# Performance work log

Hardware: AMD Instinct MI355X
Metric: run time of the kernel (lower is better)

## Reference

```python
import jax, jax.numpy as jnp
import numpy as np

N = 50000   # nodes per graph
F = 128     # num_features (== hidden width 128 in GCNConv stack)
G = 3       # number_graphs
E = 600000  # edges per graph


def setup_inputs() -> dict:
    key = jax.random.key(0)
    ks = jax.random.split(key, 16)
    s = 0.05  # glorot-ish scale for 128-wide layers
    inp = {
        "x": jax.random.normal(ks[0], (G, N, F), jnp.float32),
        "fc1_w": jax.random.normal(ks[1], (G, F, F), jnp.float32) * s,
        "fc1_b": jnp.zeros((G, F), jnp.float32),
        "w_conv1": jax.random.normal(ks[2], (F, 128), jnp.float32) * s,
        "b_conv1": jnp.zeros((128,), jnp.float32),
        "w_conv2": jax.random.normal(ks[3], (128, 128), jnp.float32) * s,
        "b_conv2": jnp.zeros((128,), jnp.float32),
        "w_dconv1": jax.random.normal(ks[4], (128, 128), jnp.float32) * s,
        "b_dconv1": jnp.zeros((128,), jnp.float32),
        "w_dconv2": jax.random.normal(ks[5], (128, F), jnp.float32) * s,
        "b_dconv2": jnp.zeros((F,), jnp.float32),
        "fc2_w": jax.random.normal(ks[6], (2 * F, F), jnp.float32) * s,
        "fc2_b": jnp.zeros((F,), jnp.float32),
        "att_w": jax.random.normal(ks[7], (G, 128, 128), jnp.float32) * s,
        "edge_index": jax.random.randint(ks[8], (G, 2, E), 0, N, jnp.int64),
    }
    return inp


def _gcn(x, src, dst, W, b):
    # PyG GCNConv: add self-loops, symmetric D^-1/2 (A+I) D^-1/2 normalization
    n = x.shape[0]
    h = x @ W                                  # [N, out]
    loops = jnp.arange(n)
    s = jnp.concatenate([src, loops])
    d = jnp.concatenate([dst, loops])
    deg = jax.ops.segment_sum(jnp.ones_like(d, dtype=h.dtype), d, num_segments=n)
    dinv = jnp.where(deg > 0, jax.lax.rsqrt(deg), 0.0)
    norm = dinv[s] * dinv[d]                   # [E+N]
    out = jax.ops.segment_sum(h[s] * norm[:, None], d, num_segments=n)
    return out + b


_gcn_g = jax.vmap(_gcn, in_axes=(0, 0, 0, None, None))  # over graphs (shared weights)


def _fro(a):
    # Frobenius norm over last two axes (matches torch.norm(., p=2) on a matrix)
    return jnp.sqrt(jnp.sum(a * a, axis=(-2, -1)))


def reference(x, fc1_w, fc1_b, w_conv1, b_conv1, w_conv2, b_conv2,
              w_dconv1, b_dconv1, w_dconv2, b_dconv2, fc2_w, fc2_b,
              att_w, edge_index):
    g = x.shape[0]
    src, dst = edge_index[:, 0], edge_index[:, 1]

    # per-graph fc1 (distinct weights per graph)
    pre_feat = jnp.einsum('gnf,gfo->gno', x, fc1_w) + fc1_b[:, None, :]
    conv1_f = _gcn_g(pre_feat, src, dst, w_conv1, b_conv1)   # [G,N,128]
    enc = _gcn_g(conv1_f, src, dst, w_conv2, b_conv2)        # encoder_H [G,N,128]

    global_vec = jax.nn.sigmoid(jnp.mean(enc, axis=1))       # [G,128]

    # leave-one-out decoder input: (sum_j enc_j - enc_i) / (G-1)
    dec_in = (jnp.sum(enc, axis=0)[None] - enc) / (g - 1)

    own1 = _gcn_g(enc, src, dst, w_dconv1, b_dconv1)         # decov1_f
    own2 = _gcn_g(own1, src, dst, w_dconv2, b_dconv2)        # reconstructed x
    oth1 = _gcn_g(dec_in, src, dst, w_dconv1, b_dconv1)
    oth2 = _gcn_g(oth1, src, dst, w_dconv2, b_dconv2)

    fuse_h = jnp.concatenate([own2, oth2], axis=-1)          # [G,N,2F]
    each_fin = jnp.einsum('gnf,fo->gno', fuse_h, fc2_w) + fc2_b  # [G,N,F]

    # cross-graph attention: sigmoid(H_j @ W_i @ g_i) for all (i, j)
    u = jnp.einsum('ide,ie->id', att_w, global_vec)          # W_i @ g_i -> [G,128]
    S = jax.nn.sigmoid(jnp.einsum('jnd,id->ijn', enc, u))    # [i,j,n]
    L = jnp.transpose(S, (0, 2, 1))                          # [i,n,j]
    L = L / jnp.sum(L, axis=-1, keepdims=True)               # row-normalize over j
    comp_re = jnp.transpose(L, (1, 0, 2)).reshape(x.shape[1], g * g)  # [N, G*G]

    fuse_feat = jax.nn.sigmoid(jnp.mean(each_fin, axis=0))   # [N,F]
    used_feat = jax.nn.elu(jnp.mean(enc, axis=0))            # [N,128]

    obf1 = jnp.sum((_fro(pre_feat - own2) + _fro(conv1_f - own1)) / 2)
    obf0 = jnp.float32(0.0)
    for i in range(g):
        for j in range(g):
            if i != j:
                obf0 = obf0 + _fro(each_fin[i] - each_fin[j])
    return (fuse_feat, used_feat, comp_re, obf1, obf0)
```

## Files before the change

kernel.cpp:

```cpp
#include <hip/hip_runtime.h>

#define NN 50000
#define NFEAT 128
#define NG 3
#define NE 600000

typedef unsigned int u32;
typedef unsigned short u16;
typedef __bf16 bf16x8 __attribute__((ext_vector_type(8)));
typedef float f32x4 __attribute__((ext_vector_type(4)));

__device__ __forceinline__ u16 f2bf(float f){
  u32 u = __float_as_uint(f);
  return (u16)((u + 0x7fffu + ((u >> 16) & 1u)) >> 16);
}
__device__ __forceinline__ float bf2f(u32 s){
  return __uint_as_float((s & 0xffffu) << 16);
}
__device__ __forceinline__ u32 pack2(float a, float b){
  return (u32)f2bf(a) | ((u32)f2bf(b) << 16);
}
__device__ __forceinline__ float sigm(float x){ return 1.f / (1.f + __expf(-x)); }

__global__ void wprep_kernel(const float* fc1w, const float* wc1, const float* wc2,
                             const float* wd1, const float* wd2, const float* fc2w,
                             u16* WT){
  int idx = blockIdx.x * 256 + threadIdx.x;
  if (idx >= 147456) return;
  float v;
  if (idx < 49152){
    int g = idx / 16384, r = idx % 16384; int o = r / 128, f = r % 128;
    v = fc1w[g * 16384 + f * 128 + o];
  } else if (idx < 114688){
    int m = (idx - 49152) / 16384, r = (idx - 49152) % 16384;
    int o = r / 128, f = r % 128;
    const float* w = (m == 0) ? wc1 : (m == 1) ? wc2 : (m == 2) ? wd1 : wd2;
    v = w[f * 128 + o];
  } else {
    int r = idx - 114688; int half = r / 16384; r %= 16384;
    int o = r / 128, f = r % 128;
    v = fc2w[(half * 128 + f) * 128 + o];
  }
  WT[idx] = f2bf(v);
}

__global__ void deg_kernel(const int* ei, int* deg){
  int t = blockIdx.x * 256 + threadIdx.x;
  if (t >= NG * NE) return;
  int g = t / NE, e = t - g * NE;
  int dst = ei[(size_t)g * 2 * NE + NE + e];
  atomicAdd(deg + (size_t)g * NN + dst, 1);
}

__global__ __launch_bounds__(1024) void scan_kernel(const int* deg, int* rowptr, float* dinv){
  const int g = blockIdx.x;
  const int* d = deg + (size_t)g * NN;
  int* rp = rowptr + g * (NN + 1);
  float* di = dinv + (size_t)g * NN;
  __shared__ int s[1024];
  __shared__ int carry;
  if (threadIdx.x == 0) carry = 0;
  __syncthreads();
  for (int base = 0; base <= NN; base += 1024){
    int idx = base + threadIdx.x;
    int v = (idx < NN) ? d[idx] : 0;
    if (idx < NN) di[idx] = rsqrtf((float)(v + 1));
    s[threadIdx.x] = v;
    __syncthreads();
    for (int off = 1; off < 1024; off <<= 1){
      int x = (threadIdx.x >= off) ? s[threadIdx.x - off] : 0;
      __syncthreads();
      s[threadIdx.x] += x;
      __syncthreads();
    }
    int incl = s[threadIdx.x];
    int run = carry;
    if (idx <= NN) rp[idx] = run + incl - v;
    __syncthreads();
    if (threadIdx.x == 1023) carry = run + s[1023];
    __syncthreads();
  }
}

__global__ void fill_kernel(const int* ei, const int* rowptr, int* cursor, int* colbuf){
  int t = blockIdx.x * 256 + threadIdx.x;
  if (t >= NG * NE) return;
  int g = t / NE, e = t - g * NE;
  int src = ei[(size_t)g * 2 * NE + e];
  int dst = ei[(size_t)g * 2 * NE + NE + e];
  int pos = atomicAdd(cursor + (size_t)g * NN + dst, 1);
  colbuf[(size_t)g * NE + rowptr[g * (NN + 1) + dst] + pos] = src;
}

template<int MODE>
__global__ __launch_bounds__(256, 2) void gemm_kernel(
    const void* Ap, const void* Ap2, const u16* W, const u16* W2,
    const float* bias, u16* Out, int wPerG, int biasPerG, int hasBias)
{
  __shared__ __align__(16) unsigned char sA[128 * 256];
  __shared__ __align__(16) unsigned char sW[128 * 256];
  const int tid = threadIdx.x;
  const int g = blockIdx.y;
  const int nb = blockIdx.x * 128;
  const int lane = tid & 63, wv = tid >> 6;
  const int wm = (wv & 1) * 64, wn = (wv >> 1) * 64;
  const int l15 = lane & 15, lh = lane >> 4;
  f32x4 acc[4][4] = {};
  constexpr int passes = (MODE == 3) ? 2 : 1;
  for (int p = 0; p < passes; p++){
    if (p) __syncthreads();
    {
      const u16* wsrc = (p ? W2 : W) + (wPerG ? g * 16384 : 0);
      const uint4* w4 = (const uint4*)wsrc;
      for (int i = tid; i < 2048; i += 256){
        int r = i >> 4, c = i & 15;
        uint4 v = w4[i];
        *(uint4*)(sW + r * 256 + ((c * 16) ^ ((r & 7) << 4))) = v;
      }
    }
    if (MODE == 1){
      const float* xp = (const float*)Ap + (size_t)g * NN * NFEAT;
      for (int i = tid; i < 2048; i += 256){
        int r = i >> 4, c = i & 15; int node = nb + r;
        uint4 o = {0, 0, 0, 0};
        if (node < NN){
          const float* row = xp + (size_t)node * NFEAT + c * 8;
          float4 a4 = *(const float4*)row;
          float4 b4 = *(const float4*)(row + 4);
          o.x = pack2(a4.x, a4.y); o.y = pack2(a4.z, a4.w);
          o.z = pack2(b4.x, b4.y); o.w = pack2(b4.z, b4.w);
        }
        *(uint4*)(sA + r * 256 + ((c * 16) ^ ((r & 7) << 4))) = o;
      }
    } else if (MODE == 2){
      const uint4* pe = (const uint4*)((const u16*)Ap + (size_t)g * NN * NFEAT);
      const uint4* ps = (const uint4*)Ap2;
      for (int i = tid; i < 2048; i += 256){
        int r = i >> 4, c = i & 15; int node = nb + r;
        uint4 o = {0, 0, 0, 0};
        if (node < NN){
          uint4 va = pe[(size_t)node * 16 + c];
          uint4 vb = ps[(size_t)node * 16 + c];
          o.x = pack2(0.5f * (bf2f(vb.x) - bf2f(va.x)), 0.5f * (bf2f(vb.x >> 16) - bf2f(va.x >> 16)));
          o.y = pack2(0.5f * (bf2f(vb.y) - bf2f(va.y)), 0.5f * (bf2f(vb.y >> 16) - bf2f(va.y >> 16)));
          o.z = pack2(0.5f * (bf2f(vb.z) - bf2f(va.z)), 0.5f * (bf2f(vb.z >> 16) - bf2f(va.z >> 16)));
          o.w = pack2(0.5f * (bf2f(vb.w) - bf2f(va.w)), 0.5f * (bf2f(vb.w >> 16) - bf2f(va.w >> 16)));
        }
        *(uint4*)(sA + r * 256 + ((c * 16) ^ ((r & 7) << 4))) = o;
      }
    } else {
      const u16* asrc = (const u16*)(p ? Ap2 : Ap) + (size_t)g * NN * NFEAT;
      const uint4* a4 = (const uint4*)asrc;
      for (int i = tid; i < 2048; i += 256){
        int r = i >> 4, c = i & 15; int node = nb + r;
        uint4 v = {0, 0, 0, 0};
        if (node < NN) v = a4[(size_t)node * 16 + c];
        *(uint4*)(sA + r * 256 + ((c * 16) ^ ((r & 7) << 4))) = v;
      }
    }
    __syncthreads();
    #pragma unroll
    for (int k0 = 0; k0 < 128; k0 += 32){
      const int kb = 2 * (k0 + lh * 8);
      bf16x8 af[4], bfr[4];
      #pragma unroll
      for (int t = 0; t < 4; t++){
        int rm = wm + t * 16 + l15;
        af[t] = *reinterpret_cast<const bf16x8*>(sW + rm * 256 + (kb ^ ((rm & 7) << 4)));
        int rn = wn + t * 16 + l15;
        bfr[t] = *reinterpret_cast<const bf16x8*>(sA + rn * 256 + (kb ^ ((rn & 7) << 4)));
      }
      #pragma unroll
      for (int mi = 0; mi < 4; mi++)
        #pragma unroll
        for (int ni = 0; ni < 4; ni++)
          acc[mi][ni] = __builtin_amdgcn_mfma_f32_16x16x32_bf16(af[mi], bfr[ni], acc[mi][ni], 0, 0, 0);
    }
  }
  u16* outg = Out + (size_t)g * NN * NFEAT;
  #pragma unroll
  for (int mi = 0; mi < 4; mi++){
    int mbase = wm + mi * 16 + lh * 4;
    f32x4 bv = {};
    if (hasBias) bv = *reinterpret_cast<const f32x4*>(bias + (biasPerG ? g * NFEAT : 0) + mbase);
    #pragma unroll
    for (int ni = 0; ni < 4; ni++){
      int node = nb + wn + ni * 16 + l15;
      if (node < NN){
        f32x4 v = acc[mi][ni];
        ushort4 o;
        o.x = f2bf(v.x + bv.x); o.y = f2bf(v.y + bv.y);
        o.z = f2bf(v.z + bv.z); o.w = f2bf(v.w + bv.w);
        *reinterpret_cast<ushort4*>(outg + (size_t)node * NFEAT + mbase) = o;
      }
    }
  }
}

template<bool SQ>
__global__ __launch_bounds__(256) void agg_kernel(
    const u16* H, u16* Outp, const float* bias, const float* dinv,
    const int* rowptr, const int* colidx, const u16* Ref, float* sqslot)
{
  __shared__ float red[256];
  const int g = blockIdx.y;
  const int v = blockIdx.x * 4 + (threadIdx.x >> 6);
  const int l = threadIdx.x & 63;
  const u32* h = (const u32*)(H + (size_t)g * NN * NFEAT);
  const float* dv = dinv + (size_t)g * NN;
  const int* rp = rowptr + g * (NN + 1);
  const int* ci = colidx + (size_t)g * NE;
  float ax = 0.f, ay = 0.f;
  const int e0 = rp[v], e1 = rp[v + 1];
  int e = e0;
  for (; e + 1 < e1; e += 2){
    int s0 = ci[e], s1 = ci[e + 1];
    float w0 = dv[s0], w1 = dv[s1];
    u32 h0 = h[(size_t)s0 * 64 + l], h1 = h[(size_t)s1 * 64 + l];
    ax += w0 * bf2f(h0) + w1 * bf2f(h1);
    ay += w0 * bf2f(h0 >> 16) + w1 * bf2f(h1 >> 16);
  }
  if (e < e1){
    int s0 = ci[e]; float w0 = dv[s0];
    u32 h0 = h[(size_t)s0 * 64 + l];
    ax += w0 * bf2f(h0); ay += w0 * bf2f(h0 >> 16);
  }
  const float dvv = dv[v];
  u32 hs = h[(size_t)v * 64 + l];
  ax = (ax + dvv * bf2f(hs)) * dvv;
  ay = (ay + dvv * bf2f(hs >> 16)) * dvv;
  const float2 b2 = *(const float2*)(bias + 2 * l);
  ax += b2.x; ay += b2.y;
  ((u32*)(Outp + (size_t)g * NN * NFEAT))[(size_t)v * 64 + l] = pack2(ax, ay);
  if (SQ){
    u32 rv = ((const u32*)(Ref + (size_t)g * NN * NFEAT))[(size_t)v * 64 + l];
    float dx = bf2f(rv) - ax, dy = bf2f(rv >> 16) - ay;
    red[threadIdx.x] = dx * dx + dy * dy;
    __syncthreads();
    for (int s2 = 128; s2 > 0; s2 >>= 1){
      if (threadIdx.x < s2) red[threadIdx.x] += red[threadIdx.x + s2];
      __syncthreads();
    }
    if (threadIdx.x == 0) atomicAdd(sqslot + g, red[0]);
  }
}

__global__ __launch_bounds__(256) void encsum_kernel(
    const u16* Enc, u16* EncSum, float* outUsed, float* colsum)
{
  const int fp = threadIdx.x & 63, sub = threadIdx.x >> 6;
  const u32* e0 = (const u32*)Enc;
  const u32* e1 = e0 + (size_t)NN * 64;
  const u32* e2 = e1 + (size_t)NN * 64;
  u32* es = (u32*)EncSum;
  float cs[6] = {0, 0, 0, 0, 0, 0};
  for (int v = blockIdx.x * 4 + sub; v < NN; v += gridDim.x * 4){
    size_t idx = (size_t)v * 64 + fp;
    u32 a = e0[idx], b = e1[idx], c = e2[idx];
    float axv = bf2f(a), ayv = bf2f(a >> 16);
    float bxv = bf2f(b), byv = bf2f(b >> 16);
    float cxv = bf2f(c), cyv = bf2f(c >> 16);
    cs[0] += axv; cs[1] += ayv; cs[2] += bxv; cs[3] += byv; cs[4] += cxv; cs[5] += cyv;
    float sx = axv + bxv + cxv, sy = ayv + byv + cyv;
    es[idx] = pack2(sx, sy);
    float ux = sx * (1.f / 3.f), uy = sy * (1.f / 3.f);
    float2 o;
    o.x = ux > 0.f ? ux : expm1f(ux);
    o.y = uy > 0.f ? uy : expm1f(uy);
    *(float2*)(outUsed + (size_t)v * NFEAT + 2 * fp) = o;
  }
  __shared__ float red[256];
  #pragma unroll
  for (int q = 0; q < 6; q++){
    red[threadIdx.x] = cs[q];
    __syncthreads();
    if (sub == 0){
      float s = red[fp] + red[64 + fp] + red[128 + fp] + red[192 + fp];
      atomicAdd(&colsum[(q >> 1) * NFEAT + 2 * fp + (q & 1)], s);
    }
    __syncthreads();
  }
}

__global__ void gvecu_kernel(const float* colsum, const float* att, float* u){
  __shared__ float gv[3 * 128];
  const int t = threadIdx.x;
  for (int g = 0; g < 3; g++) gv[g * 128 + t] = sigm(colsum[g * 128 + t] * (1.f / 50000.f));
  __syncthreads();
  for (int i = 0; i < 3; i++){
    float s = 0.f;
    for (int e = 0; e < 128; e++)
      s += att[(size_t)i * 16384 + (size_t)t * 128 + e] * gv[i * 128 + e];
    u[i * 128 + t] = s;
  }
}

__global__ __launch_bounds__(256) void fuse_kernel(const u16* EF, float* outFuse, float* slots){
  const int fp = threadIdx.x & 63, sub = threadIdx.x >> 6;
  const u32* e0 = (const u32*)EF;
  const u32* e1 = e0 + (size_t)NN * 64;
  const u32* e2 = e1 + (size_t)NN * 64;
  float s01 = 0, s02 = 0, s12 = 0;
  for (int v = blockIdx.x * 4 + sub; v < NN; v += gridDim.x * 4){
    size_t idx = (size_t)v * 64 + fp;
    u32 a = e0[idx], b = e1[idx], c = e2[idx];
    float axv = bf2f(a), ayv = bf2f(a >> 16), bxv = bf2f(b), byv = bf2f(b >> 16);
    float cxv = bf2f(c), cyv = bf2f(c >> 16);
    float2 o;
    o.x = sigm((axv + bxv + cxv) * (1.f / 3.f));
    o.y = sigm((ayv + byv + cyv) * (1.f / 3.f));
    *(float2*)(outFuse + (size_t)v * NFEAT + 2 * fp) = o;
    float dx, dy;
    dx = axv - bxv; dy = ayv - byv; s01 += dx * dx + dy * dy;
    dx = axv - cxv; dy = ayv - cyv; s02 += dx * dx + dy * dy;
    dx = bxv - cxv; dy = byv - cyv; s12 += dx * dx + dy * dy;
  }
  __shared__ float red[256];
  float vals[3] = {s01, s02, s12};
  #pragma unroll
  for (int q = 0; q < 3; q++){
    red[threadIdx.x] = vals[q];
    __syncthreads();
    for (int s2 = 128; s2 > 0; s2 >>= 1){
      if (threadIdx.x < s2) red[threadIdx.x] += red[threadIdx.x + s2];
      __syncthreads();
    }
    if (threadIdx.x == 0) atomicAdd(slots + 6 + q, red[0]);
    __syncthreads();
  }
}

__global__ __launch_bounds__(256) void comp_kernel(const u16* Enc, const float* u, float* outC){
  __shared__ float su[384];
  for (int i = threadIdx.x; i < 384; i += 256) su[i] = u[i];
  __syncthreads();
  const int v = blockIdx.x * 4 + (threadIdx.x >> 6);
  const int l = threadIdx.x & 63;
  const u32* e = (const u32*)Enc;
  float ex[3], ey[3];
  #pragma unroll
  for (int j = 0; j < 3; j++){
    u32 t = e[((size_t)j * NN + v) * 64 + l];
    ex[j] = bf2f(t); ey[j] = bf2f(t >> 16);
  }
  float p[9];
  #pragma unroll
  for (int i = 0; i < 3; i++){
    float uxi = su[i * 128 + 2 * l], uyi = su[i * 128 + 2 * l + 1];
    #pragma unroll
    for (int j = 0; j < 3; j++)
      p[i * 3 + j] = ex[j] * uxi + ey[j] * uyi;
  }
  #pragma unroll
  for (int q = 0; q < 9; q++){
    float s = p[q];
    #pragma unroll
    for (int off = 1; off < 64; off <<= 1) s += __shfl_xor(s, off, 64);
    p[q] = s;
  }
  if (l < 9){
    float sg[9];
    #pragma unroll
    for (int q = 0; q < 9; q++) sg[q] = sigm(p[q]);
    float d0 = sg[0] + sg[1] + sg[2], d1 = sg[3] + sg[4] + sg[5], d2 = sg[6] + sg[7] + sg[8];
    float num = sg[0];
    if (l == 1) num = sg[1]; if (l == 2) num = sg[2]; if (l == 3) num = sg[3];
    if (l == 4) num = sg[4]; if (l == 5) num = sg[5]; if (l == 6) num = sg[6];
    if (l == 7) num = sg[7]; if (l == 8) num = sg[8];
    float den = (l < 3) ? d0 : (l < 6) ? d1 : d2;
    outC[(size_t)v * 9 + l] = num / den;
  }
}

__global__ void final_kernel(const float* slots, float* out){
  if (threadIdx.x == 0){
    float obf1 = 0.f;
    for (int g = 0; g < 3; g++)
      obf1 += 0.5f * (sqrtf(slots[3 + g]) + sqrtf(slots[g]));
    float obf0 = 2.f * (sqrtf(slots[6]) + sqrtf(slots[7]) + sqrtf(slots[8]));
    out[13250000] = obf1;
    out[13250001] = obf0;
  }
}

extern "C" void kernel_launch(void* const* d_in, const int* in_sizes, int n_in,
                              void* d_out, int out_size, void* d_ws, size_t ws_size,
                              hipStream_t stream)
{
  (void)in_sizes; (void)n_in; (void)out_size;
  const float* x    = (const float*)d_in[0];
  const float* fc1w = (const float*)d_in[1];
  const float* fc1b = (const float*)d_in[2];
  const float* wc1  = (const float*)d_in[3];
  const float* bc1  = (const float*)d_in[4];
  const float* wc2  = (const float*)d_in[5];
  const float* bc2  = (const float*)d_in[6];
  const float* wd1  = (const float*)d_in[7];
  const float* bd1  = (const float*)d_in[8];
  const float* wd2  = (const float*)d_in[9];
  const float* bd2  = (const float*)d_in[10];
  const float* fc2w = (const float*)d_in[11];
  const float* fc2b = (const float*)d_in[12];
  const float* attw = (const float*)d_in[13];
  const int*   ei   = (const int*)d_in[14];
  float* out = (float*)d_out;
  char* ws = (char*)d_ws;

  constexpr size_t BUFB = (size_t)NG * NN * NFEAT * 2;
  u16* WT   = (u16*)(ws + 0);
  u16* buf0 = (u16*)(ws + 327680);
  u16* buf1 = (u16*)(ws + 327680 + 1 * BUFB);
  u16* buf2 = (u16*)(ws + 327680 + 2 * BUFB);
  u16* buf3 = (u16*)(ws + 327680 + 3 * BUFB);
  u16* buf4 = (u16*)(ws + 327680 + 4 * BUFB);
  u16* buf5 = (u16*)(ws + 327680 + 5 * BUFB);
  size_t off = 327680 + 6 * BUFB;
  u16* encsum = (u16*)(ws + off); off += (size_t)NN * NFEAT * 2;
  float* dinv = (float*)(ws + off); off += (size_t)NG * NN * 4;
  int* rowptr = (int*)(ws + off); off += 600064;
  int* colbuf = (int*)(ws + off); off += (size_t)NG * NE * 4;
  size_t zero_off = off;
  int* deg     = (int*)(ws + off); off += (size_t)NG * NN * 4;
  int* cursor  = (int*)(ws + off); off += (size_t)NG * NN * 4;
  float* colsum = (float*)(ws + off); off += 1536;
  float* slots  = (float*)(ws + off); off += 64;
  size_t zero_bytes = off - zero_off;
  float* uvec = (float*)(ws + off); off += 1536;
  if (ws_size < off) return;

  hipMemsetAsync(ws + zero_off, 0, zero_bytes, stream);

  wprep_kernel<<<576, 256, 0, stream>>>(fc1w, wc1, wc2, wd1, wd2, fc2w, WT);
  deg_kernel<<<7032, 256, 0, stream>>>(ei, deg);
  scan_kernel<<<NG, 1024, 0, stream>>>(deg, rowptr, dinv);
  fill_kernel<<<7032, 256, 0, stream>>>(ei, rowptr, cursor, colbuf);

  const u16* WT_fc1 = WT;
  const u16* WT_c1  = WT + 49152;
  const u16* WT_c2  = WT + 65536;
  const u16* WT_d1  = WT + 81920;
  const u16* WT_d2  = WT + 98304;
  const u16* WT_f2a = WT + 114688;
  const u16* WT_f2b = WT + 131072;
  dim3 gg(391, NG), ag(12500, NG);

  gemm_kernel<1><<<gg, 256, 0, stream>>>(x, nullptr, WT_fc1, nullptr, fc1b, buf0, 1, 1, 1);
  gemm_kernel<0><<<gg, 256, 0, stream>>>(buf0, nullptr, WT_c1, nullptr, nullptr, buf3, 0, 0, 0);
  agg_kernel<false><<<ag, 256, 0, stream>>>(buf3, buf1, bc1, dinv, rowptr, colbuf, nullptr, nullptr);
  gemm_kernel<0><<<gg, 256, 0, stream>>>(buf1, nullptr, WT_c2, nullptr, nullptr, buf3, 0, 0, 0);
  agg_kernel<false><<<ag, 256, 0, stream>>>(buf3, buf2, bc2, dinv, rowptr, colbuf, nullptr, nullptr);
  encsum_kernel<<<256, 256, 0, stream>>>(buf2, encsum, out + 6400000, colsum);
  gvecu_kernel<<<1, 128, 0, stream>>>(colsum, attw, uvec);
  gemm_kernel<0><<<gg, 256, 0, stream>>>(buf2, nullptr, WT_d1, nullptr, nullptr, buf3, 0, 0, 0);
  agg_kernel<true><<<ag, 256, 0, stream>>>(buf3, buf4, bd1, dinv, rowptr, colbuf, buf1, slots + 0);
  gemm_kernel<0><<<gg, 256, 0, stream>>>(buf4, nullptr, WT_d2, nullptr, nullptr, buf3, 0, 0, 0);
  agg_kernel<true><<<ag, 256, 0, stream>>>(buf3, buf5, bd2, dinv, rowptr, colbuf, buf0, slots + 3);
  gemm_kernel<2><<<gg, 256, 0, stream>>>(buf2, encsum, WT_d1, nullptr, nullptr, buf3, 0, 0, 0);
  agg_kernel<false><<<ag, 256, 0, stream>>>(buf3, buf1, bd1, dinv, rowptr, colbuf, nullptr, nullptr);
  gemm_kernel<0><<<gg, 256, 0, stream>>>(buf1, nullptr, WT_d2, nullptr, nullptr, buf3, 0, 0, 0);
  agg_kernel<false><<<ag, 256, 0, stream>>>(buf3, buf4, bd2, dinv, rowptr, colbuf, nullptr, nullptr);
  gemm_kernel<3><<<gg, 256, 0, stream>>>(buf5, buf4, WT_f2a, WT_f2b, fc2b, buf0, 0, 0, 1);
  fuse_kernel<<<256, 256, 0, stream>>>(buf0, out, slots);
  comp_kernel<<<12500, 256, 0, stream>>>(buf2, uvec, out + 12800000);
  final_kernel<<<1, 64, 0, stream>>>(slots, out);
}
```

Measured before the change: 2.235 ms.

## Pre-scale GEMM output by source dinv and vectorize edge aggregation with uint4 gathers

The GEMM epilogue now multiplies each node's row by its dinv, so the aggregation kernel no longer gathers a per-edge dinv[src] weight and only sums pre-scaled rows. The aggregation is restructured so each wavefront processes 8 neighbours at a time, with 16 lanes per row reading uint4 (8 bf16) chunks, followed by a cross-lane shuffle reduction. The SQ reduction uses wave shuffles and a 4-entry shared array instead of a full 256-entry tree. This trades an extra bf16 rounding of pre-scaled values and some idle lanes on low-degree nodes for fewer dependent loads and wider memory transactions.

```diff
diff --git a/kernel.cpp b/kernel.cpp
--- a/kernel.cpp
+++ b/kernel.cpp
@@ -95,7 +95,8 @@
 template<int MODE>
 __global__ __launch_bounds__(256, 2) void gemm_kernel(
     const void* Ap, const void* Ap2, const u16* W, const u16* W2,
-    const float* bias, u16* Out, int wPerG, int biasPerG, int hasBias)
+    const float* bias, u16* Out, const float* scale,
+    int wPerG, int biasPerG, int hasBias)
 {
   __shared__ __align__(16) unsigned char sA[128 * 256];
   __shared__ __align__(16) unsigned char sW[128 * 256];
@@ -177,6 +178,15 @@
           acc[mi][ni] = __builtin_amdgcn_mfma_f32_16x16x32_bf16(af[mi], bfr[ni], acc[mi][ni], 0, 0, 0);
     }
   }
+  float scn[4] = {1.f, 1.f, 1.f, 1.f};
+  if (scale){
+    const float* sg = scale + (size_t)g * NN;
+    #pragma unroll
+    for (int ni = 0; ni < 4; ni++){
+      int node = nb + wn + ni * 16 + l15;
+      scn[ni] = (node < NN) ? sg[node] : 0.f;
+    }
+  }
   u16* outg = Out + (size_t)g * NN * NFEAT;
   #pragma unroll
   for (int mi = 0; mi < 4; mi++){
@@ -188,9 +198,10 @@
       int node = nb + wn + ni * 16 + l15;
       if (node < NN){
         f32x4 v = acc[mi][ni];
+        float s = scn[ni];
         ushort4 o;
-        o.x = f2bf(v.x + bv.x); o.y = f2bf(v.y + bv.y);
-        o.z = f2bf(v.z + bv.z); o.w = f2bf(v.w + bv.w);
+        o.x = f2bf((v.x + bv.x) * s); o.y = f2bf((v.y + bv.y) * s);
+        o.z = f2bf((v.z + bv.z) * s); o.w = f2bf((v.w + bv.w) * s);
         *reinterpret_cast<ushort4*>(outg + (size_t)node * NFEAT + mbase) = o;
       }
     }
@@ -202,46 +213,75 @@
     const u16* H, u16* Outp, const float* bias, const float* dinv,
     const int* rowptr, const int* colidx, const u16* Ref, float* sqslot)
 {
-  __shared__ float red[256];
   const int g = blockIdx.y;
   const int v = blockIdx.x * 4 + (threadIdx.x >> 6);
   const int l = threadIdx.x & 63;
-  const u32* h = (const u32*)(H + (size_t)g * NN * NFEAT);
-  const float* dv = dinv + (size_t)g * NN;
+  const int q = l >> 4, sub = l & 15;
+  const uint4* h4 = (const uint4*)(H + (size_t)g * NN * NFEAT);
   const int* rp = rowptr + g * (NN + 1);
   const int* ci = colidx + (size_t)g * NE;
-  float ax = 0.f, ay = 0.f;
-  const int e0 = rp[v], e1 = rp[v + 1];
-  int e = e0;
-  for (; e + 1 < e1; e += 2){
-    int s0 = ci[e], s1 = ci[e + 1];
-    float w0 = dv[s0], w1 = dv[s1];
-    u32 h0 = h[(size_t)s0 * 64 + l], h1 = h[(size_t)s1 * 64 + l];
-    ax += w0 * bf2f(h0) + w1 * bf2f(h1);
-    ay += w0 * bf2f(h0 >> 16) + w1 * bf2f(h1 >> 16);
-  }
-  if (e < e1){
-    int s0 = ci[e]; float w0 = dv[s0];
-    u32 h0 = h[(size_t)s0 * 64 + l];
-    ax += w0 * bf2f(h0); ay += w0 * bf2f(h0 >> 16);
-  }
-  const float dvv = dv[v];
-  u32 hs = h[(size_t)v * 64 + l];
-  ax = (ax + dvv * bf2f(hs)) * dvv;
-  ay = (ay + dvv * bf2f(hs >> 16)) * dvv;
-  const float2 b2 = *(const float2*)(bias + 2 * l);
-  ax += b2.x; ay += b2.y;
-  ((u32*)(Outp + (size_t)g * NN * NFEAT))[(size_t)v * 64 + l] = pack2(ax, ay);
+  const int e0 = rp[v];
+  const int nslot = rp[v + 1] - e0 + 1;
+  float a0=0,a1=0,a2=0,a3=0,a4=0,a5=0,a6=0,a7=0;
+  const int nIter = (nslot + 7) >> 3;
+  for (int it = 0; it < nIter; ++it){
+    int sA = it * 8 + q;
+    int sB = sA + 4;
+    int srcA = (sA == 0) ? v : ((sA < nslot) ? ci[e0 + sA - 1] : v);
+    int srcB = (sB < nslot) ? ci[e0 + sB - 1] : v;
+    uint4 hA = h4[(size_t)srcA * 16 + sub];
+    uint4 hB = h4[(size_t)srcB * 16 + sub];
+    if (sA < nslot){
+      a0 += bf2f(hA.x); a1 += bf2f(hA.x >> 16);
+      a2 += bf2f(hA.y); a3 += bf2f(hA.y >> 16);
+      a4 += bf2f(hA.z); a5 += bf2f(hA.z >> 16);
+      a6 += bf2f(hA.w); a7 += bf2f(hA.w >> 16);
+    }
+    if (sB < nslot){
+      a0 += bf2f(hB.x); a1 += bf2f(hB.x >> 16);
+      a2 += bf2f(hB.y); a3 += bf2f(hB.y >> 16);
+      a4 += bf2f(hB.z); a5 += bf2f(hB.z >> 16);
+      a6 += bf2f(hB.w); a7 += bf2f(hB.w >> 16);
+    }
+  }
+  a0 += __shfl_xor(a0, 16); a1 += __shfl_xor(a1, 16);
+  a2 += __shfl_xor(a2, 16); a3 += __shfl_xor(a3, 16);
+  a4 += __shfl_xor(a4, 16); a5 += __shfl_xor(a5, 16);
+  a6 += __shfl_xor(a6, 16); a7 += __shfl_xor(a7, 16);
+  a0 += __shfl_xor(a0, 32); a1 += __shfl_xor(a1, 32);
+  a2 += __shfl_xor(a2, 32); a3 += __shfl_xor(a3, 32);
+  a4 += __shfl_xor(a4, 32); a5 += __shfl_xor(a5, 32);
+  a6 += __shfl_xor(a6, 32); a7 += __shfl_xor(a7, 32);
+  const float dvv = dinv[(size_t)g * NN + v];
+  const float4 b4a = *(const float4*)(bias + sub * 8);
+  const float4 b4b = *(const float4*)(bias + sub * 8 + 4);
+  a0 = a0 * dvv + b4a.x; a1 = a1 * dvv + b4a.y;
+  a2 = a2 * dvv + b4a.z; a3 = a3 * dvv + b4a.w;
+  a4 = a4 * dvv + b4b.x; a5 = a5 * dvv + b4b.y;
+  a6 = a6 * dvv + b4b.z; a7 = a7 * dvv + b4b.w;
+  float sq = 0.f;
+  if (q == 0){
+    uint4 o;
+    o.x = pack2(a0, a1); o.y = pack2(a2, a3);
+    o.z = pack2(a4, a5); o.w = pack2(a6, a7);
+    ((uint4*)(Outp + (size_t)g * NN * NFEAT))[(size_t)v * 16 + sub] = o;
+    if (SQ){
+      uint4 rv = ((const uint4*)(Ref + (size_t)g * NN * NFEAT))[(size_t)v * 16 + sub];
+      float d;
+      d = bf2f(rv.x) - a0; sq += d * d; d = bf2f(rv.x >> 16) - a1; sq += d * d;
+      d = bf2f(rv.y) - a2; sq += d * d; d = bf2f(rv.y >> 16) - a3; sq += d * d;
+      d = bf2f(rv.z) - a4; sq += d * d; d = bf2f(rv.z >> 16) - a5; sq += d * d;
+      d = bf2f(rv.w) - a6; sq += d * d; d = bf2f(rv.w >> 16) - a7; sq += d * d;
+    }
+  }
   if (SQ){
-    u32 rv = ((const u32*)(Ref + (size_t)g * NN * NFEAT))[(size_t)v * 64 + l];
-    float dx = bf2f(rv) - ax, dy = bf2f(rv >> 16) - ay;
-    red[threadIdx.x] = dx * dx + dy * dy;
-    __syncthreads();
-    for (int s2 = 128; s2 > 0; s2 >>= 1){
-      if (threadIdx.x < s2) red[threadIdx.x] += red[threadIdx.x + s2];
-      __syncthreads();
-    }
-    if (threadIdx.x == 0) atomicAdd(sqslot + g, red[0]);
+    __shared__ float red[4];
+    sq += __shfl_xor(sq, 1); sq += __shfl_xor(sq, 2);
+    sq += __shfl_xor(sq, 4); sq += __shfl_xor(sq, 8);
+    if (l == 0) red[threadIdx.x >> 6] = sq;
+    __syncthreads();
+    if (threadIdx.x == 0)
+      atomicAdd(sqslot + g, red[0] + red[1] + red[2] + red[3]);
   }
 }
 
@@ -444,22 +484,22 @@
   const u16* WT_f2b = WT + 131072;
   dim3 gg(391, NG), ag(12500, NG);
 
-  gemm_kernel<1><<<gg, 256, 0, stream>>>(x, nullptr, WT_fc1, nullptr, fc1b, buf0, 1, 1, 1);
-  gemm_kernel<0><<<gg, 256, 0, stream>>>(buf0, nullptr, WT_c1, nullptr, nullptr, buf3, 0, 0, 0);
+  gemm_kernel<1><<<gg, 256, 0, stream>>>(x, nullptr, WT_fc1, nullptr, fc1b, buf0, nullptr, 1, 1, 1);
+  gemm_kernel<0><<<gg, 256, 0, stream>>>(buf0, nullptr, WT_c1, nullptr, nullptr, buf3, dinv, 0, 0, 0);
   agg_kernel<false><<<ag, 256, 0, stream>>>(buf3, buf1, bc1, dinv, rowptr, colbuf, nullptr, nullptr);
-  gemm_kernel<0><<<gg, 256, 0, stream>>>(buf1, nullptr, WT_c2, nullptr, nullptr, buf3, 0, 0, 0);
+  gemm_kernel<0><<<gg, 256, 0, stream>>>(buf1, nullptr, WT_c2, nullptr, nullptr, buf3, dinv, 0, 0, 0);
   agg_kernel<false><<<ag, 256, 0, stream>>>(buf3, buf2, bc2, dinv, rowptr, colbuf, nullptr, nullptr);
   encsum_kernel<<<256, 256, 0, stream>>>(buf2, encsum, out + 6400000, colsum);
   gvecu_kernel<<<1, 128, 0, stream>>>(colsum, attw, uvec);
-  gemm_kernel<0><<<gg, 256, 0, stream>>>(buf2, nullptr, WT_d1, nullptr, nullptr, buf3, 0, 0, 0);
+  gemm_kernel<0><<<gg, 256, 0, stream>>>(buf2, nullptr, WT_d1, nullptr, nullptr, buf3, dinv, 0, 0, 0);
   agg_kernel<true><<<ag, 256, 0, stream>>>(buf3, buf4, bd1, dinv, rowptr, colbuf, buf1, slots + 0);
-  gemm_kernel<0><<<gg, 256, 0, stream>>>(buf4, nullptr, WT_d2, nullptr, nullptr, buf3, 0, 0, 0);
+  gemm_kernel<0><<<gg, 256, 0, stream>>>(buf4, nullptr, WT_d2, nullptr, nullptr, buf3, dinv, 0, 0, 0);
   agg_kernel<true><<<ag, 256, 0, stream>>>(buf3, buf5, bd2, dinv, rowptr, colbuf, buf0, slots + 3);
-  gemm_kernel<2><<<gg, 256, 0, stream>>>(buf2, encsum, WT_d1, nullptr, nullptr, buf3, 0, 0, 0);
+  gemm_kernel<2><<<gg, 256, 0, stream>>>(buf2, encsum, WT_d1, nullptr, nullptr, buf3, dinv, 0, 0, 0);
   agg_kernel<false><<<ag, 256, 0, stream>>>(buf3, buf1, bd1, dinv, rowptr, colbuf, nullptr, nullptr);
-  gemm_kernel<0><<<gg, 256, 0, stream>>>(buf1, nullptr, WT_d2, nullptr, nullptr, buf3, 0, 0, 0);
+  gemm_kernel<0><<<gg, 256, 0, stream>>>(buf1, nullptr, WT_d2, nullptr, nullptr, buf3, dinv, 0, 0, 0);
   agg_kernel<false><<<ag, 256, 0, stream>>>(buf3, buf4, bd2, dinv, rowptr, colbuf, nullptr, nullptr);
-  gemm_kernel<3><<<gg, 256, 0, stream>>>(buf5, buf4, WT_f2a, WT_f2b, fc2b, buf0, 0, 0, 1);
+  gemm_kernel<3><<<gg, 256, 0, stream>>>(buf5, buf4, WT_f2a, WT_f2b, fc2b, buf0, nullptr, 0, 0, 1);
   fuse_kernel<<<256, 256, 0, stream>>>(buf0, out, slots);
   comp_kernel<<<12500, 256, 0, stream>>>(buf2, uvec, out + 12800000);
   final_kernel<<<1, 64, 0, stream>>>(slots, out);
```

Result: faster. 2.078 ms (-7.0%).
